# Optimization experiments

Measured on AMD Instinct MI355X. Metric: run time of the kernel, lower is better.

## Reference

```python
import jax, jax.numpy as jnp
import numpy as np
import math

B, L, D, H, NT, T, NLAYERS = 64, 128, 512, 8, 10000, 65536, 2
DH = D // H
FF = 2 * D
EPS = 1e-5


def setup_inputs() -> dict:
    key = jax.random.key(0)
    ks = jax.random.split(key, 20)
    item_ids = jax.random.randint(ks[0], (T,), 0, NT, dtype=jnp.int32)
    seg_ids = jnp.sort(jax.random.randint(ks[1], (T,), 0, B * L, dtype=jnp.int32))
    pad_mask = jnp.zeros((B, L), dtype=bool)
    future_mask = jnp.where(jnp.triu(jnp.ones((L, L), dtype=bool), k=1), -1e9, 0.0).astype(jnp.float32)

    s = 0.02
    emb = (jax.random.normal(ks[2], (NT + 1, D), jnp.float32) * s).at[NT].set(0.0)  # padding_idx row is zero
    Wqkv = jax.random.normal(ks[3], (NLAYERS, 3 * D, D), jnp.float32) * s
    bqkv = jnp.zeros((NLAYERS, 3 * D), jnp.float32)
    Wo = jax.random.normal(ks[4], (NLAYERS, D, D), jnp.float32) * s
    bo = jnp.zeros((NLAYERS, D), jnp.float32)
    W1 = jax.random.normal(ks[5], (NLAYERS, FF, D), jnp.float32) * s
    b1 = jnp.zeros((NLAYERS, FF), jnp.float32)
    W2 = jax.random.normal(ks[6], (NLAYERS, D, FF), jnp.float32) * s
    b2 = jnp.zeros((NLAYERS, D), jnp.float32)
    ln1_s = jnp.ones((NLAYERS, D), jnp.float32)
    ln1_b = jnp.zeros((NLAYERS, D), jnp.float32)
    ln2_s = jnp.ones((NLAYERS, D), jnp.float32)
    ln2_b = jnp.zeros((NLAYERS, D), jnp.float32)
    Wout = jax.random.normal(ks[7], (NT, D), jnp.float32) * s
    bout = jnp.zeros((NT,), jnp.float32)
    return dict(item_ids=item_ids, seg_ids=seg_ids, pad_mask=pad_mask, future_mask=future_mask,
                max_len=L, emb=emb, Wqkv=Wqkv, bqkv=bqkv, Wo=Wo, bo=bo, W1=W1, b1=b1, W2=W2, b2=b2,
                ln1_s=ln1_s, ln1_b=ln1_b, ln2_s=ln2_s, ln2_b=ln2_b, Wout=Wout, bout=bout)


def _layernorm(x, s, b):
    m = jnp.mean(x, axis=-1, keepdims=True)
    v = jnp.mean(jnp.square(x - m), axis=-1, keepdims=True)
    return (x - m) * jax.lax.rsqrt(v + EPS) * s + b


def _pos_encoding(maxlen, d):
    den = jnp.exp(-jnp.arange(0, d, 2, dtype=jnp.float32) * (math.log(10000.0) / d))
    pos = jnp.arange(maxlen, dtype=jnp.float32)[:, None]
    pe = jnp.zeros((maxlen, d), jnp.float32)
    pe = pe.at[:, 0::2].set(jnp.sin(pos * den))
    pe = pe.at[:, 1::2].set(jnp.cos(pos * den))
    return pe


def reference(item_ids, seg_ids, pad_mask, future_mask, max_len, emb,
              Wqkv, bqkv, Wo, bo, W1, b1, W2, b2, ln1_s, ln1_b, ln2_s, ln2_b, Wout, bout):
    # fused gather + segment-mean (replaces the per-user Python loops)
    counts = jax.ops.segment_sum(jnp.ones((T,), jnp.float32), seg_ids, num_segments=B * max_len)
    sums = jax.ops.segment_sum(emb[item_ids], seg_ids, num_segments=B * max_len)  # [B*L, D]
    means = jnp.where(counts[:, None] > 0, sums / jnp.maximum(counts, 1.0)[:, None], 0.0)
    x = means.reshape(B, max_len, D) + _pos_encoding(max_len, D)

    key_mask = jnp.where(pad_mask[:, None, None, :], -1e9, 0.0)  # [B,1,1,L]
    scale = 1.0 / math.sqrt(DH)
    for i in range(NLAYERS):
        qkv = x @ Wqkv[i].T + bqkv[i]                         # [B,L,3D]
        q, k, v = jnp.split(qkv, 3, axis=-1)
        q = q.reshape(B, max_len, H, DH)
        k = k.reshape(B, max_len, H, DH)
        v = v.reshape(B, max_len, H, DH)
        scores = jnp.einsum('bqhd,bkhd->bhqk', q, k) * scale + future_mask + key_mask
        attn = jax.nn.softmax(scores, axis=-1)
        o = jnp.einsum('bhqk,bkhd->bqhd', attn, v).reshape(B, max_len, D)
        o = o @ Wo[i].T + bo[i]
        x = _layernorm(x + o, ln1_s[i], ln1_b[i])              # post-norm
        ff = jax.nn.relu(x @ W1[i].T + b1[i]) @ W2[i].T + b2[i]
        x = _layernorm(x + ff, ln2_s[i], ln2_b[i])
    return x @ Wout.T + bout  # [B, L, num_types]
```

## Files before the change

kernel.cpp:

```cpp
#include <hip/hip_runtime.h>

#define T_TOTAL 65536
#define SEQ 128
#define DMODEL 512
#define DHEAD 64
#define NTYPES 10000
#define ROWS 8192
#define NOUT_PAD 10112

typedef float floatx4 __attribute__((ext_vector_type(4)));
typedef short shortx8 __attribute__((ext_vector_type(8)));

#define GLOAD_LDS(gp, lp) __builtin_amdgcn_global_load_lds( \
    (const __attribute__((address_space(1))) void*)(gp),    \
    (__attribute__((address_space(3))) void*)(lp), 16, 0, 0)

__device__ __forceinline__ unsigned short f2bf(float f) {
  union { float f; unsigned u; } v; v.f = f;
  unsigned u = v.u + 0x7fffu + ((v.u >> 16) & 1u);
  return (unsigned short)(u >> 16);
}

__global__ __launch_bounds__(256) void convert_pad_kernel(
    const float* __restrict__ src, unsigned short* __restrict__ dst,
    long nsrc, long ndst) {
  long i = (long)blockIdx.x * 1024 + (long)threadIdx.x * 4;
  if (i >= ndst) return;
  float4 v = make_float4(0.f, 0.f, 0.f, 0.f);
  if (i < nsrc) v = *(const float4*)(src + i);
  ushort4 o;
  o.x = f2bf(v.x); o.y = f2bf(v.y); o.z = f2bf(v.z); o.w = f2bf(v.w);
  *(ushort4*)(dst + i) = o;
}

__global__ __launch_bounds__(128) void seg_mean_kernel(
    const int* __restrict__ item_ids, const int* __restrict__ seg_ids,
    const float* __restrict__ emb, float* __restrict__ x_f,
    unsigned short* __restrict__ x_b) {
  int s = blockIdx.x;
  int lo = 0, hi = T_TOTAL;
  while (lo < hi) { int mid = (lo + hi) >> 1; if (seg_ids[mid] < s) lo = mid + 1; else hi = mid; }
  int start = lo;
  hi = T_TOTAL;
  while (lo < hi) { int mid = (lo + hi) >> 1; if (seg_ids[mid] <= s) lo = mid + 1; else hi = mid; }
  int end = lo;
  int c = threadIdx.x << 2;
  float4 acc = make_float4(0.f, 0.f, 0.f, 0.f);
  for (int j = start; j < end; ++j) {
    const float* e = emb + (long)item_ids[j] * DMODEL + c;
    float4 v = *(const float4*)e;
    acc.x += v.x; acc.y += v.y; acc.z += v.z; acc.w += v.w;
  }
  int cnt = end - start;
  float inv = cnt > 0 ? 1.0f / (float)cnt : 0.0f;
  float mv[4] = {acc.x * inv, acc.y * inv, acc.z * inv, acc.w * inv};
  int l = s & (SEQ - 1);
  const float klog = 0.017988946039015984f;
  long base = (long)s * DMODEL + c;
#pragma unroll
  for (int t = 0; t < 4; ++t) {
    int col = c + t;
    float den = expf(-(float)(col & ~1) * klog);
    float ang = (float)l * den;
    float pe = (col & 1) ? cosf(ang) : sinf(ang);
    float val = mv[t] + pe;
    x_f[base + t] = val;
    x_b[base + t] = f2bf(val);
  }
}

__global__ __launch_bounds__(256) void gemm_bt_kernel(
    const unsigned short* __restrict__ A,
    const unsigned short* __restrict__ B,
    const float* __restrict__ bias,
    float* __restrict__ Cf,
    unsigned short* __restrict__ Cb,
    int K, int Nreal, int ldC, int relu) {
  __shared__ unsigned short As[128 * 32];
  __shared__ unsigned short Bs[128 * 32];
  const int tid = threadIdx.x;
  const int lane = tid & 63;
  const int wave = tid >> 6;
  const int wm = (wave >> 1) << 6;
  const int wn = (wave & 1) << 6;
  const int l16 = lane & 15;
  const int quad = lane >> 4;
  const long rowA0 = (long)blockIdx.x * 128;
  const long rowB0 = (long)blockIdx.y * 128;

  floatx4 acc[4][4] = {};

  const int rowOff = tid >> 2;
  const int kOff = (tid & 3) << 3;
  const unsigned short* gA = A + (rowA0 + rowOff) * (long)K + kOff;
  const unsigned short* gB = B + (rowB0 + rowOff) * (long)K + kOff;
  unsigned short* lA = As + tid * 8;
  unsigned short* lB = Bs + tid * 8;

  for (int k0 = 0; k0 < K; k0 += 32) {
    __syncthreads();
    GLOAD_LDS(gA + k0, lA);
    GLOAD_LDS(gA + 64 * (long)K + k0, lA + 2048);
    GLOAD_LDS(gB + k0, lB);
    GLOAD_LDS(gB + 64 * (long)K + k0, lB + 2048);
    __syncthreads();
    shortx8 af[4], bfr[4];
#pragma unroll
    for (int i = 0; i < 4; ++i)
      af[i] = *(const shortx8*)(As + (wm + i * 16 + l16) * 32 + quad * 8);
#pragma unroll
    for (int j = 0; j < 4; ++j)
      bfr[j] = *(const shortx8*)(Bs + (wn + j * 16 + l16) * 32 + quad * 8);
#pragma unroll
    for (int i = 0; i < 4; ++i)
#pragma unroll
      for (int j = 0; j < 4; ++j)
        acc[i][j] = __builtin_amdgcn_mfma_f32_16x16x32_bf16(af[i], bfr[j], acc[i][j], 0, 0, 0);
  }

#pragma unroll
  for (int i = 0; i < 4; ++i) {
    int row = (int)rowA0 + wm + i * 16 + quad * 4;
#pragma unroll
    for (int j = 0; j < 4; ++j) {
      int col = (int)rowB0 + wn + j * 16 + l16;
      if (col < Nreal) {
        float bv = bias ? bias[col] : 0.0f;
#pragma unroll
        for (int r = 0; r < 4; ++r) {
          float v = acc[i][j][r] + bv;
          if (relu) v = fmaxf(v, 0.0f);
          long off = (long)(row + r) * ldC + col;
          if (Cf) Cf[off] = v;
          if (Cb) Cb[off] = f2bf(v);
        }
      }
    }
  }
}

__global__ __launch_bounds__(128) void attn_kernel(
    const float* __restrict__ qkv,
    unsigned short* __restrict__ o_b) {
  __shared__ float Ks[SEQ * DHEAD];
  __shared__ float Vs[SEQ * DHEAD];
  int b = blockIdx.x >> 3, h = blockIdx.x & 7;
  const float* base = qkv + (long)b * SEQ * 1536;
  int hoff = h * DHEAD;
  for (int idx = threadIdx.x; idx < SEQ * DHEAD; idx += 128) {
    int l = idx >> 6, c = idx & 63;
    Ks[idx] = base[l * 1536 + 512 + hoff + c];
    Vs[idx] = base[l * 1536 + 1024 + hoff + c];
  }
  __syncthreads();
  int l = threadIdx.x;
  float q[DHEAD];
#pragma unroll
  for (int c = 0; c < DHEAD; ++c) q[c] = base[l * 1536 + hoff + c];
  float o[DHEAD];
#pragma unroll
  for (int c = 0; c < DHEAD; ++c) o[c] = 0.f;
  float denom = 0.f;
  for (int j = 0; j <= l; ++j) {
    const float* kr = Ks + j * DHEAD;
    float s0 = 0.f, s1 = 0.f, s2 = 0.f, s3 = 0.f;
#pragma unroll
    for (int c = 0; c < DHEAD; c += 4) {
      s0 += q[c] * kr[c];     s1 += q[c + 1] * kr[c + 1];
      s2 += q[c + 2] * kr[c + 2]; s3 += q[c + 3] * kr[c + 3];
    }
    float p = __expf(((s0 + s1) + (s2 + s3)) * 0.125f);
    denom += p;
    const float* vr = Vs + j * DHEAD;
#pragma unroll
    for (int c = 0; c < DHEAD; ++c) o[c] += p * vr[c];
  }
  float inv = 1.0f / denom;
  unsigned short* dst = o_b + ((long)b * SEQ + l) * DMODEL + hoff;
#pragma unroll
  for (int c = 0; c < DHEAD; ++c) dst[c] = f2bf(o[c] * inv);
}

__global__ __launch_bounds__(256) void add_ln_kernel(
    const float* __restrict__ x_in, const float* __restrict__ delta,
    const float* __restrict__ gamma, const float* __restrict__ beta,
    float* __restrict__ x_f, unsigned short* __restrict__ x_b) {
  int row = blockIdx.x;
  int tid = threadIdx.x;
  long base = (long)row * DMODEL;
  int c = tid * 2;
  float2 xv = *(const float2*)(x_in + base + c);
  float2 dv = *(const float2*)(delta + base + c);
  float a = xv.x + dv.x, b = xv.y + dv.y;
  float s = a + b;
  float sq = a * a + b * b;
#pragma unroll
  for (int off = 32; off > 0; off >>= 1) {
    s += __shfl_down(s, off, 64);
    sq += __shfl_down(sq, off, 64);
  }
  __shared__ float red[8];
  __shared__ float mean_s, rstd_s;
  int wv = tid >> 6, ln = tid & 63;
  if (ln == 0) { red[wv] = s; red[4 + wv] = sq; }
  __syncthreads();
  if (tid == 0) {
    float S = red[0] + red[1] + red[2] + red[3];
    float SQ = red[4] + red[5] + red[6] + red[7];
    float mean = S * (1.0f / 512.0f);
    float var = SQ * (1.0f / 512.0f) - mean * mean;
    mean_s = mean;
    rstd_s = rsqrtf(var + 1e-5f);
  }
  __syncthreads();
  float mean = mean_s, rstd = rstd_s;
  float o0 = (a - mean) * rstd * gamma[c] + beta[c];
  float o1 = (b - mean) * rstd * gamma[c + 1] + beta[c + 1];
  x_f[base + c] = o0;
  x_f[base + c + 1] = o1;
  x_b[base + c] = f2bf(o0);
  x_b[base + c + 1] = f2bf(o1);
}

extern "C" void kernel_launch(void* const* d_in, const int* in_sizes, int n_in,
                              void* d_out, int out_size, void* d_ws, size_t ws_size,
                              hipStream_t stream) {
  const int* item_ids = (const int*)d_in[0];
  const int* seg_ids = (const int*)d_in[1];
  const float* emb  = (const float*)d_in[5];
  const float* Wqkv = (const float*)d_in[6];
  const float* bqkv = (const float*)d_in[7];
  const float* Wo   = (const float*)d_in[8];
  const float* bo   = (const float*)d_in[9];
  const float* W1   = (const float*)d_in[10];
  const float* b1   = (const float*)d_in[11];
  const float* W2   = (const float*)d_in[12];
  const float* b2   = (const float*)d_in[13];
  const float* ln1s = (const float*)d_in[14];
  const float* ln1b = (const float*)d_in[15];
  const float* ln2s = (const float*)d_in[16];
  const float* ln2b = (const float*)d_in[17];
  const float* Wout = (const float*)d_in[18];
  const float* bout = (const float*)d_in[19];
  float* out = (float*)d_out;

  char* ws = (char*)d_ws;
  size_t off = 0;
  auto alloc = [&](size_t bytes) {
    void* p = ws + off;
    off += (bytes + 255) & ~(size_t)255;
    return p;
  };
  float* x_f  = (float*)alloc((size_t)ROWS * 512 * 4);
  unsigned short* x_b = (unsigned short*)alloc((size_t)ROWS * 512 * 2);
  float* qkv_f = (float*)alloc((size_t)ROWS * 1536 * 4);
  unsigned short* o_b = (unsigned short*)alloc((size_t)ROWS * 512 * 2);
  float* tmp_f = (float*)alloc((size_t)ROWS * 512 * 4);
  unsigned short* h_b = (unsigned short*)alloc((size_t)ROWS * 1024 * 2);
  unsigned short* wqkv_b = (unsigned short*)alloc((size_t)2 * 1536 * 512 * 2);
  unsigned short* wo_b = (unsigned short*)alloc((size_t)2 * 512 * 512 * 2);
  unsigned short* w1_b = (unsigned short*)alloc((size_t)2 * 1024 * 512 * 2);
  unsigned short* w2_b = (unsigned short*)alloc((size_t)2 * 512 * 1024 * 2);
  unsigned short* wout_b = (unsigned short*)alloc((size_t)NOUT_PAD * 512 * 2);

  auto cvt = [&](const float* src, unsigned short* dst, long nsrc, long ndst) {
    unsigned blocks = (unsigned)((ndst + 1023) / 1024);
    convert_pad_kernel<<<blocks, 256, 0, stream>>>(src, dst, nsrc, ndst);
  };
  cvt(Wqkv, wqkv_b, 2L * 1536 * 512, 2L * 1536 * 512);
  cvt(Wo, wo_b, 2L * 512 * 512, 2L * 512 * 512);
  cvt(W1, w1_b, 2L * 1024 * 512, 2L * 1024 * 512);
  cvt(W2, w2_b, 2L * 512 * 1024, 2L * 512 * 1024);
  cvt(Wout, wout_b, (long)NTYPES * 512, (long)NOUT_PAD * 512);

  seg_mean_kernel<<<ROWS, 128, 0, stream>>>(item_ids, seg_ids, emb, x_f, x_b);

  for (int i = 0; i < 2; ++i) {
    gemm_bt_kernel<<<dim3(64, 12), 256, 0, stream>>>(
        x_b, wqkv_b + (long)i * 1536 * 512, bqkv + i * 1536,
        qkv_f, nullptr, 512, 1536, 1536, 0);
    attn_kernel<<<512, 128, 0, stream>>>(qkv_f, o_b);
    gemm_bt_kernel<<<dim3(64, 4), 256, 0, stream>>>(
        o_b, wo_b + (long)i * 512 * 512, bo + i * 512,
        tmp_f, nullptr, 512, 512, 512, 0);
    add_ln_kernel<<<ROWS, 256, 0, stream>>>(x_f, tmp_f, ln1s + i * 512, ln1b + i * 512, x_f, x_b);
    gemm_bt_kernel<<<dim3(64, 8), 256, 0, stream>>>(
        x_b, w1_b + (long)i * 1024 * 512, b1 + i * 1024,
        nullptr, h_b, 512, 1024, 1024, 1);
    gemm_bt_kernel<<<dim3(64, 4), 256, 0, stream>>>(
        h_b, w2_b + (long)i * 512 * 1024, b2 + i * 512,
        tmp_f, nullptr, 1024, 512, 512, 0);
    add_ln_kernel<<<ROWS, 256, 0, stream>>>(x_f, tmp_f, ln2s + i * 512, ln2b + i * 512, x_f, x_b);
  }

  gemm_bt_kernel<<<dim3(64, 79), 256, 0, stream>>>(
      x_b, wout_b, bout, out, nullptr, 512, NTYPES, NTYPES, 0);
}
```

Baseline: 960.3 us.

## Add 256x256 double-buffered MFMA GEMM and split attention keys across two thread halves

```diff
diff --git a/kernel.cpp b/kernel.cpp
--- a/kernel.cpp
+++ b/kernel.cpp
@@ -6,7 +6,7 @@
 #define DHEAD 64
 #define NTYPES 10000
 #define ROWS 8192
-#define NOUT_PAD 10112
+#define NOUT_PAD 10240
 
 typedef float floatx4 __attribute__((ext_vector_type(4)));
 typedef short shortx8 __attribute__((ext_vector_type(8)));
@@ -14,11 +14,19 @@
 #define GLOAD_LDS(gp, lp) __builtin_amdgcn_global_load_lds( \
     (const __attribute__((address_space(1))) void*)(gp),    \
     (__attribute__((address_space(3))) void*)(lp), 16, 0, 0)
+
+#define MFMA_BF16 __builtin_amdgcn_mfma_f32_16x16x32_bf16
 
 __device__ __forceinline__ unsigned short f2bf(float f) {
   union { float f; unsigned u; } v; v.f = f;
   unsigned u = v.u + 0x7fffu + ((v.u >> 16) & 1u);
   return (unsigned short)(u >> 16);
+}
+
+__device__ __forceinline__ void phase_barrier() {
+  __builtin_amdgcn_sched_barrier(0);
+  __builtin_amdgcn_s_barrier();
+  __builtin_amdgcn_sched_barrier(0);
 }
 
 __global__ __launch_bounds__(256) void convert_pad_kernel(
@@ -115,7 +123,7 @@
     for (int i = 0; i < 4; ++i)
 #pragma unroll
       for (int j = 0; j < 4; ++j)
-        acc[i][j] = __builtin_amdgcn_mfma_f32_16x16x32_bf16(af[i], bfr[j], acc[i][j], 0, 0, 0);
+        acc[i][j] = MFMA_BF16(af[i], bfr[j], acc[i][j], 0, 0, 0);
   }
 
 #pragma unroll
@@ -139,21 +147,183 @@
   }
 }
 
-__global__ __launch_bounds__(128) void attn_kernel(
+__global__ __launch_bounds__(512, 2) void gemm256_kernel(
+    const unsigned short* __restrict__ A,
+    const unsigned short* __restrict__ B,
+    const float* __restrict__ bias,
+    float* __restrict__ Cf,
+    unsigned short* __restrict__ Cb,
+    int K, int Nreal, int ldC, int relu) {
+  __shared__ unsigned short As[2][256 * 64];
+  __shared__ unsigned short Bs[2][256 * 64];
+  const int tid = threadIdx.x;
+  const int lane = tid & 63;
+  const int wave = tid >> 6;
+  const int wm = wave >> 2;
+  const int wn = wave & 3;
+  const int l16 = lane & 15;
+  const int quad = lane >> 4;
+  const long rowA0 = (long)blockIdx.x * 256;
+  const long rowB0 = (long)blockIdx.y * 256;
+
+  floatx4 acc[8][4] = {};
+
+  const int srow = tid >> 3;
+  const int scol = (tid & 7) << 3;
+  const unsigned short* gA = A + (rowA0 + srow) * (long)K + scol;
+  const unsigned short* gB = B + (rowB0 + srow) * (long)K + scol;
+  const int loff = tid * 8;
+  const long rstep = 64 * (long)K;
+
+#pragma unroll
+  for (int is = 0; is < 4; ++is) {
+    GLOAD_LDS(gA + is * rstep, &As[0][is * 4096 + loff]);
+    GLOAD_LDS(gB + is * rstep, &Bs[0][is * 4096 + loff]);
+  }
+  asm volatile("s_waitcnt vmcnt(0)" ::: "memory");
+  phase_barrier();
+
+  const int KT = K >> 6;
+  for (int kt = 0; kt < KT; ++kt) {
+    const int cur = kt & 1;
+    const unsigned short* Ab = As[cur];
+    const unsigned short* Bb = Bs[cur];
+    unsigned short* An = As[cur ^ 1];
+    unsigned short* Bn = Bs[cur ^ 1];
+    const bool stage = (kt + 1) < KT;
+    const unsigned short* gAn = gA + (long)(kt + 1) * 64;
+    const unsigned short* gBn = gB + (long)(kt + 1) * 64;
+
+    shortx8 af[4][2], bf[4][2];
+
+#pragma unroll
+    for (int m = 0; m < 4; ++m) {
+      const unsigned short* p = Ab + (wm * 128 + m * 16 + l16) * 64 + quad * 8;
+      af[m][0] = *(const shortx8*)(p);
+      af[m][1] = *(const shortx8*)(p + 32);
+    }
+#pragma unroll
+    for (int n = 0; n < 2; ++n) {
+      const unsigned short* p = Bb + (wn * 64 + n * 16 + l16) * 64 + quad * 8;
+      bf[n][0] = *(const shortx8*)(p);
+      bf[n][1] = *(const shortx8*)(p + 32);
+    }
+    if (stage) {
+      GLOAD_LDS(gAn, An + loff);
+      GLOAD_LDS(gAn + rstep, An + 4096 + loff);
+    }
+    phase_barrier();
+    __builtin_amdgcn_s_setprio(1);
+#pragma unroll
+    for (int m = 0; m < 4; ++m)
+#pragma unroll
+      for (int n = 0; n < 2; ++n) {
+        acc[m][n] = MFMA_BF16(af[m][0], bf[n][0], acc[m][n], 0, 0, 0);
+        acc[m][n] = MFMA_BF16(af[m][1], bf[n][1], acc[m][n], 0, 0, 0);
+      }
+    __builtin_amdgcn_s_setprio(0);
+    phase_barrier();
+
+#pragma unroll
+    for (int n = 2; n < 4; ++n) {
+      const unsigned short* p = Bb + (wn * 64 + n * 16 + l16) * 64 + quad * 8;
+      bf[n][0] = *(const shortx8*)(p);
+      bf[n][1] = *(const shortx8*)(p + 32);
+    }
+    if (stage) {
+      GLOAD_LDS(gAn + 2 * rstep, An + 8192 + loff);
+      GLOAD_LDS(gAn + 3 * rstep, An + 12288 + loff);
+    }
+    phase_barrier();
+    __builtin_amdgcn_s_setprio(1);
+#pragma unroll
+    for (int m = 0; m < 4; ++m)
+#pragma unroll
+      for (int n = 2; n < 4; ++n) {
+        acc[m][n] = MFMA_BF16(af[m][0], bf[n][0], acc[m][n], 0, 0, 0);
+        acc[m][n] = MFMA_BF16(af[m][1], bf[n][1], acc[m][n], 0, 0, 0);
+      }
+    __builtin_amdgcn_s_setprio(0);
+    phase_barrier();
+
+#pragma unroll
+    for (int m = 0; m < 4; ++m) {
+      const unsigned short* p = Ab + (wm * 128 + 64 + m * 16 + l16) * 64 + quad * 8;
+      af[m][0] = *(const shortx8*)(p);
+      af[m][1] = *(const shortx8*)(p + 32);
+    }
+    if (stage) {
+      GLOAD_LDS(gBn, Bn + loff);
+      GLOAD_LDS(gBn + rstep, Bn + 4096 + loff);
+    }
+    phase_barrier();
+    __builtin_amdgcn_s_setprio(1);
+#pragma unroll
+    for (int m = 0; m < 4; ++m)
+#pragma unroll
+      for (int n = 0; n < 2; ++n) {
+        acc[4 + m][n] = MFMA_BF16(af[m][0], bf[n][0], acc[4 + m][n], 0, 0, 0);
+        acc[4 + m][n] = MFMA_BF16(af[m][1], bf[n][1], acc[4 + m][n], 0, 0, 0);
+      }
+    __builtin_amdgcn_s_setprio(0);
+    phase_barrier();
+
+    if (stage) {
+      GLOAD_LDS(gBn + 2 * rstep, Bn + 8192 + loff);
+      GLOAD_LDS(gBn + 3 * rstep, Bn + 12288 + loff);
+    }
+    phase_barrier();
+    __builtin_amdgcn_s_setprio(1);
+#pragma unroll
+    for (int m = 0; m < 4; ++m)
+#pragma unroll
+      for (int n = 2; n < 4; ++n) {
+        acc[4 + m][n] = MFMA_BF16(af[m][0], bf[n][0], acc[4 + m][n], 0, 0, 0);
+        acc[4 + m][n] = MFMA_BF16(af[m][1], bf[n][1], acc[4 + m][n], 0, 0, 0);
+      }
+    __builtin_amdgcn_s_setprio(0);
+    asm volatile("s_waitcnt vmcnt(0)" ::: "memory");
+    phase_barrier();
+  }
+
+#pragma unroll
+  for (int m = 0; m < 8; ++m) {
+    int row = (int)rowA0 + wm * 128 + m * 16 + quad * 4;
+#pragma unroll
+    for (int n = 0; n < 4; ++n) {
+      int col = (int)rowB0 + wn * 64 + n * 16 + l16;
+      if (col < Nreal) {
+        float bv = bias ? bias[col] : 0.0f;
+#pragma unroll
+        for (int r = 0; r < 4; ++r) {
+          float v = acc[m][n][r] + bv;
+          if (relu) v = fmaxf(v, 0.0f);
+          long off = (long)(row + r) * ldC + col;
+          if (Cf) Cf[off] = v;
+          if (Cb) Cb[off] = f2bf(v);
+        }
+      }
+    }
+  }
+}
+
+__global__ __launch_bounds__(256) void attn_kernel(
     const float* __restrict__ qkv,
     unsigned short* __restrict__ o_b) {
   __shared__ float Ks[SEQ * DHEAD];
   __shared__ float Vs[SEQ * DHEAD];
+  __shared__ float Ds[SEQ];
   int b = blockIdx.x >> 3, h = blockIdx.x & 7;
   const float* base = qkv + (long)b * SEQ * 1536;
   int hoff = h * DHEAD;
-  for (int idx = threadIdx.x; idx < SEQ * DHEAD; idx += 128) {
+  for (int idx = threadIdx.x; idx < SEQ * DHEAD; idx += 256) {
     int l = idx >> 6, c = idx & 63;
     Ks[idx] = base[l * 1536 + 512 + hoff + c];
     Vs[idx] = base[l * 1536 + 1024 + hoff + c];
   }
   __syncthreads();
-  int l = threadIdx.x;
+  int l = threadIdx.x & 127;
+  int half = threadIdx.x >> 7;
   float q[DHEAD];
 #pragma unroll
   for (int c = 0; c < DHEAD; ++c) q[c] = base[l * 1536 + hoff + c];
@@ -161,12 +331,12 @@
 #pragma unroll
   for (int c = 0; c < DHEAD; ++c) o[c] = 0.f;
   float denom = 0.f;
-  for (int j = 0; j <= l; ++j) {
+  for (int j = half; j <= l; j += 2) {
     const float* kr = Ks + j * DHEAD;
     float s0 = 0.f, s1 = 0.f, s2 = 0.f, s3 = 0.f;
 #pragma unroll
     for (int c = 0; c < DHEAD; c += 4) {
-      s0 += q[c] * kr[c];     s1 += q[c + 1] * kr[c + 1];
+      s0 += q[c] * kr[c];         s1 += q[c + 1] * kr[c + 1];
       s2 += q[c + 2] * kr[c + 2]; s3 += q[c + 3] * kr[c + 3];
     }
     float p = __expf(((s0 + s1) + (s2 + s3)) * 0.125f);
@@ -175,10 +345,22 @@
 #pragma unroll
     for (int c = 0; c < DHEAD; ++c) o[c] += p * vr[c];
   }
-  float inv = 1.0f / denom;
-  unsigned short* dst = o_b + ((long)b * SEQ + l) * DMODEL + hoff;
-#pragma unroll
-  for (int c = 0; c < DHEAD; ++c) dst[c] = f2bf(o[c] * inv);
+  __syncthreads();
+  if (half) {
+    float* os = Ks + l * DHEAD;
+#pragma unroll
+    for (int c = 0; c < DHEAD; ++c) os[c] = o[c];
+    Ds[l] = denom;
+  }
+  __syncthreads();
+  if (!half) {
+    float dtot = denom + Ds[l];
+    float inv = 1.0f / dtot;
+    const float* os = Ks + l * DHEAD;
+    unsigned short* dst = o_b + ((long)b * SEQ + l) * DMODEL + hoff;
+#pragma unroll
+    for (int c = 0; c < DHEAD; ++c) dst[c] = f2bf((o[c] + os[c]) * inv);
+  }
 }
 
 __global__ __launch_bounds__(256) void add_ln_kernel(
@@ -276,10 +458,10 @@
   seg_mean_kernel<<<ROWS, 128, 0, stream>>>(item_ids, seg_ids, emb, x_f, x_b);
 
   for (int i = 0; i < 2; ++i) {
-    gemm_bt_kernel<<<dim3(64, 12), 256, 0, stream>>>(
+    gemm256_kernel<<<dim3(32, 6), 512, 0, stream>>>(
         x_b, wqkv_b + (long)i * 1536 * 512, bqkv + i * 1536,
         qkv_f, nullptr, 512, 1536, 1536, 0);
-    attn_kernel<<<512, 128, 0, stream>>>(qkv_f, o_b);
+    attn_kernel<<<512, 256, 0, stream>>>(qkv_f, o_b);
     gemm_bt_kernel<<<dim3(64, 4), 256, 0, stream>>>(
         o_b, wo_b + (long)i * 512 * 512, bo + i * 512,
         tmp_f, nullptr, 512, 512, 512, 0);
@@ -293,6 +475,6 @@
     add_ln_kernel<<<ROWS, 256, 0, stream>>>(x_f, tmp_f, ln2s + i * 512, ln2b + i * 512, x_f, x_b);
   }
 
-  gemm_bt_kernel<<<dim3(64, 79), 256, 0, stream>>>(
+  gemm256_kernel<<<dim3(32, 40), 512, 0, stream>>>(
       x_b, wout_b, bout, out, nullptr, 512, NTYPES, NTYPES, 0);
 }
```

New measurement: 941.9 us. About the same (-1.9%).
